# Performance work log

Hardware: AMD Instinct MI355X
Metric: run time of the kernel (lower is better)

The kernel has to match this reference:

```python
import jax, jax.numpy as jnp
import numpy as np

TOPK = 16  # module init arg
EPS = 1e-12  # F.normalize eps


def setup_inputs() -> dict:
    key = jax.random.key(0)
    k1, k2, k3 = jax.random.split(key, 3)
    b, c, h, w = 2, 256, 96, 96
    rc = max(c // 4, 16)  # reduced_channels = 64
    x = jax.random.normal(k1, (b, c, h, w), dtype=jnp.float32)
    # 1x1 convs are channel-mixing matmuls; store weights as [out_ch, in_ch]
    w_reduce = jax.random.normal(k2, (rc, c), dtype=jnp.float32) * 0.05
    w_proj = jax.random.normal(k3, (c, rc), dtype=jnp.float32) * 0.05
    return {"x": x, "w_reduce": w_reduce, "w_proj": w_proj}


def reference(x, w_reduce, w_proj):
    b, c, h, w = x.shape
    n = h * w
    # reduce: 1x1 conv == channel matmul -> [b, rc, N]
    feat = jnp.einsum('rc,bchw->brhw', w_reduce, x).reshape(b, -1, n)
    # F.normalize(dim=1): divide by max(L2-norm over channels, eps)
    nrm = jnp.maximum(jnp.sqrt(jnp.sum(feat * feat, axis=1, keepdims=True)), EPS)
    nf = jnp.transpose(feat / nrm, (0, 2, 1))  # [b, N, rc]
    # cosine similarity matrix [b, N, N]
    sim = jnp.einsum('bnr,bmr->bnm', nf, nf)
    k = min(TOPK, n)
    _, idx = jax.lax.top_k(sim, k)  # [b, N, k]
    # gather top-k neighbor features and average -> [b, N, rc]
    corr = jax.vmap(lambda f, i: f[i].mean(axis=1))(nf, idx)
    # proj: 1x1 conv back to C channels, NCHW layout
    enhanced = jnp.einsum('cr,bnr->bnc', w_proj, corr)
    enhanced = jnp.transpose(enhanced, (0, 2, 1)).reshape(b, c, h, w)
    return x + enhanced
```

## Files before the change

kernel.cpp:

```cpp
#include <hip/hip_runtime.h>
#include <cstdint>
#include <cstddef>

#define NPIX 9216
#define NB 2
#define NC 256
#define RC 64
#define TK 16
#define NROWS (NB * NPIX)
#define CT 128
#define ECOLS 1152
#define NTE 9
#define MAXC 128
#define MARGIN 0.008f

typedef unsigned short ushort_t;
typedef unsigned int uint_t;
typedef __bf16 bf16x8 __attribute__((ext_vector_type(8)));
typedef float f32x4 __attribute__((ext_vector_type(4)));

__device__ __forceinline__ uint_t f2bf(float x) {
  uint_t u = __float_as_uint(x);
  return (u + 0x7FFFu + ((u >> 16) & 1u)) >> 16;
}

__device__ __forceinline__ uint_t ordu(float v) {
  uint_t u = __float_as_uint(v);
  return (u & 0x80000000u) ? ~u : (u | 0x80000000u);
}

__global__ __launch_bounds__(256) void k_reduce(
    const float* __restrict__ x, const float* __restrict__ wr,
    float* __restrict__ feat4) {
  __shared__ float wl[64 * 16];
  const int bi = blockIdx.x;
  const int pg = bi >> 4, rq = (bi >> 2) & 3, cq = bi & 3;
  const int tid = threadIdx.x;
  {
    const int cl = tid >> 2, rg = (tid & 3) * 4;
#pragma unroll
    for (int i = 0; i < 4; ++i)
      wl[cl * 16 + rg + i] = wr[(size_t)(rq * 16 + rg + i) * NC + cq * 64 + cl];
  }
  __syncthreads();

  const int p = pg * 256 + tid;
  const int b = p >= NPIX;
  const int n = p - b * NPIX;
  const float* xp = x + (size_t)b * NC * NPIX + (size_t)cq * 64 * NPIX + n;

  float4 acc[4];
#pragma unroll
  for (int i = 0; i < 4; ++i) acc[i] = make_float4(0.f, 0.f, 0.f, 0.f);

  for (int c = 0; c < 64; ++c) {
    const float xv = xp[(size_t)c * NPIX];
    const float4* w4 = (const float4*)(wl + c * 16);
#pragma unroll
    for (int i = 0; i < 4; ++i) {
      float4 w = w4[i];
      acc[i].x += w.x * xv; acc[i].y += w.y * xv;
      acc[i].z += w.z * xv; acc[i].w += w.w * xv;
    }
  }
  float4* o = (float4*)(feat4 + (((size_t)(rq * 4 + cq)) * NROWS + p) * 16);
#pragma unroll
  for (int i = 0; i < 4; ++i) o[i] = acc[i];
}

__global__ __launch_bounds__(256) void k_normsplit(
    const float* __restrict__ feat4, float* __restrict__ nf,
    ushort_t* __restrict__ hi) {
  const int t = blockIdx.x * 256 + threadIdx.x;
  const int p = t >> 2, q = t & 3;
  float4 v[4];
#pragma unroll
  for (int i = 0; i < 4; ++i) v[i] = make_float4(0.f, 0.f, 0.f, 0.f);
#pragma unroll
  for (int pt = 0; pt < 4; ++pt) {
    const float4* fp = (const float4*)(feat4 + (((size_t)(q * 4 + pt)) * NROWS + p) * 16);
#pragma unroll
    for (int i = 0; i < 4; ++i) {
      float4 a = fp[i];
      v[i].x += a.x; v[i].y += a.y; v[i].z += a.z; v[i].w += a.w;
    }
  }
  float ssq = 0.f;
#pragma unroll
  for (int i = 0; i < 4; ++i)
    ssq += v[i].x * v[i].x + v[i].y * v[i].y + v[i].z * v[i].z + v[i].w * v[i].w;
  ssq += __shfl_xor(ssq, 1);
  ssq += __shfl_xor(ssq, 2);
  const float inv = 1.f / fmaxf(sqrtf(ssq), 1e-12f);

  float s[16];
#pragma unroll
  for (int i = 0; i < 4; ++i) {
    s[i * 4 + 0] = v[i].x * inv; s[i * 4 + 1] = v[i].y * inv;
    s[i * 4 + 2] = v[i].z * inv; s[i * 4 + 3] = v[i].w * inv;
  }
  float4* no = (float4*)(nf + (size_t)p * RC + q * 16);
#pragma unroll
  for (int i = 0; i < 4; ++i)
    no[i] = make_float4(s[i * 4], s[i * 4 + 1], s[i * 4 + 2], s[i * 4 + 3]);

  uint_t hs[16];
#pragma unroll
  for (int i = 0; i < 16; ++i) hs[i] = f2bf(s[i]);
  uint4* ho = (uint4*)(hi + (size_t)p * RC + q * 16);
#pragma unroll
  for (int h = 0; h < 2; ++h)
    ho[h] = make_uint4(hs[h*8+0] | (hs[h*8+1] << 16), hs[h*8+2] | (hs[h*8+3] << 16),
                       hs[h*8+4] | (hs[h*8+5] << 16), hs[h*8+6] | (hs[h*8+7] << 16));
}

__global__ __launch_bounds__(256) void k_sim_max(
    const ushort_t* __restrict__ nf_hi, float* __restrict__ tmax) {
  __shared__ ushort_t sh[CT * 72];
  const int rb = blockIdx.x >> 3, q = blockIdx.x & 7;
  const int tid = threadIdx.x, wave = tid >> 6, lane = tid & 63;
  const int n = lane & 15, quad = lane >> 4;
  const int r0 = rb * 128 + wave * 32 + n, r1 = r0 + 16;
  const int b = rb >= 72;
  const size_t cbase = (size_t)b * NPIX;

  const bf16x8 bh00 = *(const bf16x8*)(nf_hi + (size_t)r0 * 64 + quad * 8);
  const bf16x8 bh01 = *(const bf16x8*)(nf_hi + (size_t)r0 * 64 + 32 + quad * 8);
  const bf16x8 bh10 = *(const bf16x8*)(nf_hi + (size_t)r1 * 64 + quad * 8);
  const bf16x8 bh11 = *(const bf16x8*)(nf_hi + (size_t)r1 * 64 + 32 + quad * 8);

  const int sc = tid >> 1, sseg = (tid & 1) * 32;
  float cm0 = -1e30f, cm1 = -1e30f;

  for (int t = 0; t < NTE; ++t) {
    const int cb = q * ECOLS + t * CT;
    __syncthreads();
    {
      const uint4* g = (const uint4*)(nf_hi + (cbase + cb + sc) * 64 + sseg);
      uint4* d = (uint4*)(sh + sc * 72 + sseg);
#pragma unroll
      for (int i = 0; i < 4; ++i) d[i] = g[i];
    }
    __syncthreads();

#pragma unroll 2
    for (int st = 0; st < 8; ++st) {
      const ushort_t* ap = sh + (st * 16 + n) * 72 + quad * 8;
      bf16x8 ah0 = *(const bf16x8*)ap;
      bf16x8 ah1 = *(const bf16x8*)(ap + 32);
      f32x4 z = {0.f, 0.f, 0.f, 0.f};
      f32x4 a0 = __builtin_amdgcn_mfma_f32_16x16x32_bf16(ah0, bh00, z, 0, 0, 0);
      a0 = __builtin_amdgcn_mfma_f32_16x16x32_bf16(ah1, bh01, a0, 0, 0, 0);
      f32x4 a1 = __builtin_amdgcn_mfma_f32_16x16x32_bf16(ah0, bh10, z, 0, 0, 0);
      a1 = __builtin_amdgcn_mfma_f32_16x16x32_bf16(ah1, bh11, a1, 0, 0, 0);
      cm0 = fmaxf(cm0, fmaxf(fmaxf(a0[0], a0[1]), fmaxf(a0[2], a0[3])));
      cm1 = fmaxf(cm1, fmaxf(fmaxf(a1[0], a1[1]), fmaxf(a1[2], a1[3])));
    }
    if (t % 3 == 2) {
      const int cn = t / 3;
      tmax[(size_t)r0 * 96 + (q * 4 + quad) * 3 + cn] = cm0;
      tmax[(size_t)r1 * 96 + (q * 4 + quad) * 3 + cn] = cm1;
      cm0 = -1e30f; cm1 = -1e30f;
    }
  }
}

__global__ __launch_bounds__(256) void k_thresh(
    const float* __restrict__ tmax, float* __restrict__ Tb) {
  const int wave = threadIdx.x >> 6, lane = threadIdx.x & 63;
  const int row = blockIdx.x * 4 + wave;
  const float* tp = tmax + (size_t)row * 96;
  float v0 = tp[lane];
  float v1 = (lane < 32) ? tp[64 + lane] : -1e30f;
  float m = -1e30f;
#pragma unroll
  for (int k = 0; k < TK; ++k) {
    float c = fmaxf(v0, v1);
#pragma unroll
    for (int d = 1; d < 64; d <<= 1) c = fmaxf(c, __shfl_xor(c, d));
    m = c;
    if (v0 == m) v0 = -1e30f;
    if (v1 == m) v1 = -1e30f;
  }
  if (lane == 0) Tb[row] = m - MARGIN;
}

__global__ __launch_bounds__(256) void k_collect(
    const ushort_t* __restrict__ nf_hi, const float* __restrict__ Tb,
    int* __restrict__ cidx, int* __restrict__ rowcnt) {
  __shared__ ushort_t sh[CT * 72];
  const int rb = blockIdx.x >> 3, q = blockIdx.x & 7;
  const int tid = threadIdx.x, wave = tid >> 6, lane = tid & 63;
  const int n = lane & 15, quad = lane >> 4;
  const int r0 = rb * 128 + wave * 32 + n, r1 = r0 + 16;
  const int b = rb >= 72;
  const size_t cbase = (size_t)b * NPIX;

  const bf16x8 bh00 = *(const bf16x8*)(nf_hi + (size_t)r0 * 64 + quad * 8);
  const bf16x8 bh01 = *(const bf16x8*)(nf_hi + (size_t)r0 * 64 + 32 + quad * 8);
  const bf16x8 bh10 = *(const bf16x8*)(nf_hi + (size_t)r1 * 64 + quad * 8);
  const bf16x8 bh11 = *(const bf16x8*)(nf_hi + (size_t)r1 * 64 + 32 + quad * 8);

  const float T0 = Tb[r0], T1 = Tb[r1];
  const int sc = tid >> 1, sseg = (tid & 1) * 32;

  for (int t = 0; t < NTE; ++t) {
    const int cb = q * ECOLS + t * CT;
    __syncthreads();
    {
      const uint4* g = (const uint4*)(nf_hi + (cbase + cb + sc) * 64 + sseg);
      uint4* d = (uint4*)(sh + sc * 72 + sseg);
#pragma unroll
      for (int i = 0; i < 4; ++i) d[i] = g[i];
    }
    __syncthreads();

#pragma unroll 2
    for (int st = 0; st < 8; ++st) {
      const ushort_t* ap = sh + (st * 16 + n) * 72 + quad * 8;
      bf16x8 ah0 = *(const bf16x8*)ap;
      bf16x8 ah1 = *(const bf16x8*)(ap + 32);
      f32x4 z = {0.f, 0.f, 0.f, 0.f};
      f32x4 a0 = __builtin_amdgcn_mfma_f32_16x16x32_bf16(ah0, bh00, z, 0, 0, 0);
      a0 = __builtin_amdgcn_mfma_f32_16x16x32_bf16(ah1, bh01, a0, 0, 0, 0);
      f32x4 a1 = __builtin_amdgcn_mfma_f32_16x16x32_bf16(ah0, bh10, z, 0, 0, 0);
      a1 = __builtin_amdgcn_mfma_f32_16x16x32_bf16(ah1, bh11, a1, 0, 0, 0);

      const int c0 = cb + st * 16 + quad * 4;
      const float mx0 = fmaxf(fmaxf(a0[0], a0[1]), fmaxf(a0[2], a0[3]));
      if (mx0 >= T0) {
#pragma unroll
        for (int r = 0; r < 4; ++r)
          if (a0[r] >= T0) {
            const int slot = atomicAdd(rowcnt + r0, 1);
            if (slot < MAXC) cidx[(size_t)r0 * MAXC + slot] = c0 + r;
          }
      }
      const float mx1 = fmaxf(fmaxf(a1[0], a1[1]), fmaxf(a1[2], a1[3]));
      if (mx1 >= T1) {
#pragma unroll
        for (int r = 0; r < 4; ++r)
          if (a1[r] >= T1) {
            const int slot = atomicAdd(rowcnt + r1, 1);
            if (slot < MAXC) cidx[(size_t)r1 * MAXC + slot] = c0 + r;
          }
      }
    }
  }
}

__global__ __launch_bounds__(256) void k_merge_gather(
    const float* __restrict__ nf, const int* __restrict__ cidx,
    const int* __restrict__ rowcnt, float* __restrict__ corr) {
  const int wave = threadIdx.x >> 6, lane = threadIdx.x & 63;
  const int row0 = blockIdx.x * 16 + wave * 4;
#pragma unroll 1
  for (int rr = 0; rr < 4; ++rr) {
    const int row = row0 + rr;
    const int b = row >= NPIX;
    const int rl = row - b * NPIX;
    const float* nfb = nf + (size_t)b * NPIX * RC;
    const int C = min(rowcnt[row], MAXC);

    float4 rv[16];
    const float4* r4 = (const float4*)(nf + (size_t)row * RC);
#pragma unroll
    for (int i = 0; i < 16; ++i) rv[i] = r4[i];

    const int* cp = cidx + (size_t)row * MAXC;
    unsigned long long k0 = 0, k1 = 0;
    {
      const int c0 = (lane < C) ? cp[lane] : rl;
      const float4* g = (const float4*)(nfb + (size_t)c0 * RC);
      float s = 0.f;
#pragma unroll
      for (int i = 0; i < 16; ++i) {
        float4 a = g[i];
        s += a.x * rv[i].x + a.y * rv[i].y + a.z * rv[i].z + a.w * rv[i].w;
      }
      if (lane < C)
        k0 = ((unsigned long long)ordu(s) << 32) | (uint_t)(~(uint_t)c0);
    }
    if (C > 64) {
      const int c1 = (64 + lane < C) ? cp[64 + lane] : rl;
      const float4* g = (const float4*)(nfb + (size_t)c1 * RC);
      float s = 0.f;
#pragma unroll
      for (int i = 0; i < 16; ++i) {
        float4 a = g[i];
        s += a.x * rv[i].x + a.y * rv[i].y + a.z * rv[i].z + a.w * rv[i].w;
      }
      if (64 + lane < C)
        k1 = ((unsigned long long)ordu(s) << 32) | (uint_t)(~(uint_t)c1);
    }

    int sel[TK];
#pragma unroll
    for (int t = 0; t < TK; ++t) {
      unsigned long long m = k0 > k1 ? k0 : k1;
#pragma unroll
      for (int d = 1; d < 64; d <<= 1) {
        unsigned long long o = __shfl_xor(m, d);
        m = (o > m) ? o : m;
      }
      sel[t] = (m == 0) ? rl : (int)(~(uint_t)(m & 0xFFFFFFFFull));
      if (k0 == m) k0 = 0;
      else if (k1 == m) k1 = 0;
    }

    float acc = 0.f;
#pragma unroll
    for (int t = 0; t < TK; ++t)
      acc += nfb[(size_t)sel[t] * RC + lane];
    corr[(size_t)row * RC + lane] = acc * 0.0625f;
  }
}

__global__ __launch_bounds__(256) void k_proj_add(
    const float* __restrict__ x, const float* __restrict__ wp,
    const float* __restrict__ corr, float* __restrict__ out) {
  const int pg = blockIdx.x >> 3, cq = blockIdx.x & 7;
  const int tid = threadIdx.x;

  __shared__ float wl[32 * RC];
  {
    const float4* src = (const float4*)(wp + (size_t)cq * 32 * RC);
    float4* dst = (float4*)wl;
#pragma unroll
    for (int i = 0; i < 2; ++i) dst[i * 256 + tid] = src[i * 256 + tid];
  }

  const int p = pg * 256 + tid;
  const int b = p >= NPIX;
  const int n = p - b * NPIX;

  float4 cr[16];
  const float4* c4 = (const float4*)(corr + (size_t)p * RC);
#pragma unroll
  for (int i = 0; i < 16; ++i) cr[i] = c4[i];
  __syncthreads();

  const size_t xb = (size_t)b * NC * NPIX + n;
  for (int cl = 0; cl < 32; ++cl) {
    const float4* w4 = (const float4*)(wl + cl * RC);
    float s = 0.f;
#pragma unroll
    for (int i = 0; i < 16; ++i) {
      float4 w = w4[i];
      s += w.x * cr[i].x + w.y * cr[i].y + w.z * cr[i].z + w.w * cr[i].w;
    }
    const int c = cq * 32 + cl;
    const size_t oi = xb + (size_t)c * NPIX;
    out[oi] = x[oi] + s;
  }
}

extern "C" void kernel_launch(void* const* d_in, const int* in_sizes, int n_in,
                              void* d_out, int out_size, void* d_ws, size_t ws_size,
                              hipStream_t stream) {
  const float* x = (const float*)d_in[0];
  const float* wr = (const float*)d_in[1];
  const float* wp = (const float*)d_in[2];
  float* out = (float*)d_out;

  char* ws = (char*)d_ws;
  float* feat4 = (float*)ws;
  float* tmax = (float*)ws;
  float* corr = (float*)ws;
  float* nf = (float*)(ws + 18874368);
  ushort_t* nf_hi = (ushort_t*)(ws + 23592960);
  float* Tb = (float*)(ws + 25952256);
  int* rowcnt = (int*)(ws + 26025984);
  int* cidx = (int*)(ws + 26099712);

  hipLaunchKernelGGL(k_reduce, dim3(1152), dim3(256), 0, stream, x, wr, feat4);
  hipLaunchKernelGGL(k_normsplit, dim3(288), dim3(256), 0, stream, feat4, nf, nf_hi);
  hipLaunchKernelGGL(k_sim_max, dim3(1152), dim3(256), 0, stream, nf_hi, tmax);
  hipLaunchKernelGGL(k_thresh, dim3(NROWS / 4), dim3(256), 0, stream, tmax, Tb);
  hipMemsetAsync(rowcnt, 0, NROWS * sizeof(int), stream);
  hipLaunchKernelGGL(k_collect, dim3(1152), dim3(256), 0, stream,
                     nf_hi, Tb, cidx, rowcnt);
  hipLaunchKernelGGL(k_merge_gather, dim3(1152), dim3(256), 0, stream,
                     nf, cidx, rowcnt, corr);
  hipLaunchKernelGGL(k_proj_add, dim3(576), dim3(256), 0, stream, x, wp, corr, out);
}
```

Measured before the change: 311.6 us.

## Replace atomic candidate lists with per-stripe register buffers and drop LDS staging

k_collect no longer appends candidates through global atomics into a 128-slot list per row. Each lane keeps up to four candidates in registers for its own column stripe and writes them to a fixed slot, with a byte count. This removes the rowcnt memset and the atomics. k_sim_max and k_collect now read column tiles straight from global/L2 instead of staging them in LDS with barriers, and use twice as many blocks over 576-column slices, with 192 chunk maxima per row. k_reduce computes all 64 reduced channels per thread, with merge_gather handling one row per wave over 256 possible candidates. The risk is that the per-stripe cap of four drops true top-k neighbours when many cluster in one stripe.

```diff
diff --git a/kernel.cpp b/kernel.cpp
--- a/kernel.cpp
+++ b/kernel.cpp
@@ -8,13 +8,16 @@
 #define RC 64
 #define TK 16
 #define NROWS (NB * NPIX)
-#define CT 128
-#define ECOLS 1152
-#define NTE 9
-#define MAXC 128
+#define NQ 16
+#define ECOLS 576
+#define NSUB 36
+#define NCHK 192
+#define NSTR 64
+#define CAP 4
 #define MARGIN 0.008f
 
 typedef unsigned short ushort_t;
+typedef unsigned char uchar_t;
 typedef unsigned int uint_t;
 typedef __bf16 bf16x8 __attribute__((ext_vector_type(8)));
 typedef float f32x4 __attribute__((ext_vector_type(4)));
@@ -29,43 +32,43 @@
   return (u & 0x80000000u) ? ~u : (u | 0x80000000u);
 }
 
-__global__ __launch_bounds__(256) void k_reduce(
+__global__ __launch_bounds__(128) void k_reduce(
     const float* __restrict__ x, const float* __restrict__ wr,
     float* __restrict__ feat4) {
-  __shared__ float wl[64 * 16];
+  __shared__ float wl[64 * 64];
   const int bi = blockIdx.x;
-  const int pg = bi >> 4, rq = (bi >> 2) & 3, cq = bi & 3;
+  const int pg = bi >> 2, cq = bi & 3;
   const int tid = threadIdx.x;
-  {
-    const int cl = tid >> 2, rg = (tid & 3) * 4;
-#pragma unroll
-    for (int i = 0; i < 4; ++i)
-      wl[cl * 16 + rg + i] = wr[(size_t)(rq * 16 + rg + i) * NC + cq * 64 + cl];
+#pragma unroll
+  for (int i = 0; i < 32; ++i) {
+    const int idx = i * 128 + tid;
+    const int c = idx >> 6, r = idx & 63;
+    wl[c * 64 + r] = wr[(size_t)r * NC + cq * 64 + c];
   }
   __syncthreads();
 
-  const int p = pg * 256 + tid;
+  const int p = pg * 128 + tid;
   const int b = p >= NPIX;
   const int n = p - b * NPIX;
   const float* xp = x + (size_t)b * NC * NPIX + (size_t)cq * 64 * NPIX + n;
 
-  float4 acc[4];
-#pragma unroll
-  for (int i = 0; i < 4; ++i) acc[i] = make_float4(0.f, 0.f, 0.f, 0.f);
+  float4 acc[16];
+#pragma unroll
+  for (int i = 0; i < 16; ++i) acc[i] = make_float4(0.f, 0.f, 0.f, 0.f);
 
   for (int c = 0; c < 64; ++c) {
     const float xv = xp[(size_t)c * NPIX];
-    const float4* w4 = (const float4*)(wl + c * 16);
-#pragma unroll
-    for (int i = 0; i < 4; ++i) {
+    const float4* w4 = (const float4*)(wl + c * 64);
+#pragma unroll
+    for (int i = 0; i < 16; ++i) {
       float4 w = w4[i];
       acc[i].x += w.x * xv; acc[i].y += w.y * xv;
       acc[i].z += w.z * xv; acc[i].w += w.w * xv;
     }
   }
-  float4* o = (float4*)(feat4 + (((size_t)(rq * 4 + cq)) * NROWS + p) * 16);
-#pragma unroll
-  for (int i = 0; i < 4; ++i) o[i] = acc[i];
+  float4* o = (float4*)(feat4 + ((size_t)cq * NROWS + p) * 64);
+#pragma unroll
+  for (int i = 0; i < 16; ++i) o[i] = acc[i];
 }
 
 __global__ __launch_bounds__(256) void k_normsplit(
@@ -77,8 +80,8 @@
 #pragma unroll
   for (int i = 0; i < 4; ++i) v[i] = make_float4(0.f, 0.f, 0.f, 0.f);
 #pragma unroll
-  for (int pt = 0; pt < 4; ++pt) {
-    const float4* fp = (const float4*)(feat4 + (((size_t)(q * 4 + pt)) * NROWS + p) * 16);
+  for (int cq = 0; cq < 4; ++cq) {
+    const float4* fp = (const float4*)(feat4 + ((size_t)cq * NROWS + p) * 64 + q * 16);
 #pragma unroll
     for (int i = 0; i < 4; ++i) {
       float4 a = fp[i];
@@ -116,8 +119,7 @@
 
 __global__ __launch_bounds__(256) void k_sim_max(
     const ushort_t* __restrict__ nf_hi, float* __restrict__ tmax) {
-  __shared__ ushort_t sh[CT * 72];
-  const int rb = blockIdx.x >> 3, q = blockIdx.x & 7;
+  const int rb = blockIdx.x >> 4, q = blockIdx.x & 15;
   const int tid = threadIdx.x, wave = tid >> 6, lane = tid & 63;
   const int n = lane & 15, quad = lane >> 4;
   const int r0 = rb * 128 + wave * 32 + n, r1 = r0 + 16;
@@ -129,37 +131,25 @@
   const bf16x8 bh10 = *(const bf16x8*)(nf_hi + (size_t)r1 * 64 + quad * 8);
   const bf16x8 bh11 = *(const bf16x8*)(nf_hi + (size_t)r1 * 64 + 32 + quad * 8);
 
-  const int sc = tid >> 1, sseg = (tid & 1) * 32;
   float cm0 = -1e30f, cm1 = -1e30f;
 
-  for (int t = 0; t < NTE; ++t) {
-    const int cb = q * ECOLS + t * CT;
-    __syncthreads();
-    {
-      const uint4* g = (const uint4*)(nf_hi + (cbase + cb + sc) * 64 + sseg);
-      uint4* d = (uint4*)(sh + sc * 72 + sseg);
-#pragma unroll
-      for (int i = 0; i < 4; ++i) d[i] = g[i];
-    }
-    __syncthreads();
-
-#pragma unroll 2
-    for (int st = 0; st < 8; ++st) {
-      const ushort_t* ap = sh + (st * 16 + n) * 72 + quad * 8;
-      bf16x8 ah0 = *(const bf16x8*)ap;
-      bf16x8 ah1 = *(const bf16x8*)(ap + 32);
-      f32x4 z = {0.f, 0.f, 0.f, 0.f};
-      f32x4 a0 = __builtin_amdgcn_mfma_f32_16x16x32_bf16(ah0, bh00, z, 0, 0, 0);
-      a0 = __builtin_amdgcn_mfma_f32_16x16x32_bf16(ah1, bh01, a0, 0, 0, 0);
-      f32x4 a1 = __builtin_amdgcn_mfma_f32_16x16x32_bf16(ah0, bh10, z, 0, 0, 0);
-      a1 = __builtin_amdgcn_mfma_f32_16x16x32_bf16(ah1, bh11, a1, 0, 0, 0);
-      cm0 = fmaxf(cm0, fmaxf(fmaxf(a0[0], a0[1]), fmaxf(a0[2], a0[3])));
-      cm1 = fmaxf(cm1, fmaxf(fmaxf(a1[0], a1[1]), fmaxf(a1[2], a1[3])));
-    }
-    if (t % 3 == 2) {
-      const int cn = t / 3;
-      tmax[(size_t)r0 * 96 + (q * 4 + quad) * 3 + cn] = cm0;
-      tmax[(size_t)r1 * 96 + (q * 4 + quad) * 3 + cn] = cm1;
+#pragma unroll 6
+  for (int u = 0; u < NSUB; ++u) {
+    const int col = q * ECOLS + u * 16 + n;
+    const ushort_t* ap = nf_hi + (cbase + col) * 64 + quad * 8;
+    bf16x8 ah0 = *(const bf16x8*)ap;
+    bf16x8 ah1 = *(const bf16x8*)(ap + 32);
+    f32x4 z = {0.f, 0.f, 0.f, 0.f};
+    f32x4 a0 = __builtin_amdgcn_mfma_f32_16x16x32_bf16(ah0, bh00, z, 0, 0, 0);
+    a0 = __builtin_amdgcn_mfma_f32_16x16x32_bf16(ah1, bh01, a0, 0, 0, 0);
+    f32x4 a1 = __builtin_amdgcn_mfma_f32_16x16x32_bf16(ah0, bh10, z, 0, 0, 0);
+    a1 = __builtin_amdgcn_mfma_f32_16x16x32_bf16(ah1, bh11, a1, 0, 0, 0);
+    cm0 = fmaxf(cm0, fmaxf(fmaxf(a0[0], a0[1]), fmaxf(a0[2], a0[3])));
+    cm1 = fmaxf(cm1, fmaxf(fmaxf(a1[0], a1[1]), fmaxf(a1[2], a1[3])));
+    if ((u % 12) == 11) {
+      const int cn = (q * 4 + quad) * 3 + u / 12;
+      tmax[(size_t)r0 * NCHK + cn] = cm0;
+      tmax[(size_t)r1 * NCHK + cn] = cm1;
       cm0 = -1e30f; cm1 = -1e30f;
     }
   }
@@ -169,27 +159,28 @@
     const float* __restrict__ tmax, float* __restrict__ Tb) {
   const int wave = threadIdx.x >> 6, lane = threadIdx.x & 63;
   const int row = blockIdx.x * 4 + wave;
-  const float* tp = tmax + (size_t)row * 96;
+  const float* tp = tmax + (size_t)row * NCHK;
   float v0 = tp[lane];
-  float v1 = (lane < 32) ? tp[64 + lane] : -1e30f;
+  float v1 = tp[64 + lane];
+  float v2 = tp[128 + lane];
   float m = -1e30f;
 #pragma unroll
   for (int k = 0; k < TK; ++k) {
-    float c = fmaxf(v0, v1);
+    float c = fmaxf(fmaxf(v0, v1), v2);
 #pragma unroll
     for (int d = 1; d < 64; d <<= 1) c = fmaxf(c, __shfl_xor(c, d));
     m = c;
     if (v0 == m) v0 = -1e30f;
     if (v1 == m) v1 = -1e30f;
+    if (v2 == m) v2 = -1e30f;
   }
   if (lane == 0) Tb[row] = m - MARGIN;
 }
 
 __global__ __launch_bounds__(256) void k_collect(
     const ushort_t* __restrict__ nf_hi, const float* __restrict__ Tb,
-    int* __restrict__ cidx, int* __restrict__ rowcnt) {
-  __shared__ ushort_t sh[CT * 72];
-  const int rb = blockIdx.x >> 3, q = blockIdx.x & 7;
+    ushort_t* __restrict__ cidx2, uchar_t* __restrict__ cnt2) {
+  const int rb = blockIdx.x >> 4, q = blockIdx.x & 15;
   const int tid = threadIdx.x, wave = tid >> 6, lane = tid & 63;
   const int n = lane & 15, quad = lane >> 4;
   const int r0 = rb * 128 + wave * 32 + n, r1 = r0 + 16;
@@ -202,118 +193,106 @@
   const bf16x8 bh11 = *(const bf16x8*)(nf_hi + (size_t)r1 * 64 + 32 + quad * 8);
 
   const float T0 = Tb[r0], T1 = Tb[r1];
-  const int sc = tid >> 1, sseg = (tid & 1) * 32;
-
-  for (int t = 0; t < NTE; ++t) {
-    const int cb = q * ECOLS + t * CT;
-    __syncthreads();
-    {
-      const uint4* g = (const uint4*)(nf_hi + (cbase + cb + sc) * 64 + sseg);
-      uint4* d = (uint4*)(sh + sc * 72 + sseg);
-#pragma unroll
-      for (int i = 0; i < 4; ++i) d[i] = g[i];
-    }
-    __syncthreads();
-
-#pragma unroll 2
-    for (int st = 0; st < 8; ++st) {
-      const ushort_t* ap = sh + (st * 16 + n) * 72 + quad * 8;
-      bf16x8 ah0 = *(const bf16x8*)ap;
-      bf16x8 ah1 = *(const bf16x8*)(ap + 32);
-      f32x4 z = {0.f, 0.f, 0.f, 0.f};
-      f32x4 a0 = __builtin_amdgcn_mfma_f32_16x16x32_bf16(ah0, bh00, z, 0, 0, 0);
-      a0 = __builtin_amdgcn_mfma_f32_16x16x32_bf16(ah1, bh01, a0, 0, 0, 0);
-      f32x4 a1 = __builtin_amdgcn_mfma_f32_16x16x32_bf16(ah0, bh10, z, 0, 0, 0);
-      a1 = __builtin_amdgcn_mfma_f32_16x16x32_bf16(ah1, bh11, a1, 0, 0, 0);
-
-      const int c0 = cb + st * 16 + quad * 4;
-      const float mx0 = fmaxf(fmaxf(a0[0], a0[1]), fmaxf(a0[2], a0[3]));
-      if (mx0 >= T0) {
-#pragma unroll
-        for (int r = 0; r < 4; ++r)
-          if (a0[r] >= T0) {
-            const int slot = atomicAdd(rowcnt + r0, 1);
-            if (slot < MAXC) cidx[(size_t)r0 * MAXC + slot] = c0 + r;
-          }
-      }
-      const float mx1 = fmaxf(fmaxf(a1[0], a1[1]), fmaxf(a1[2], a1[3]));
-      if (mx1 >= T1) {
-#pragma unroll
-        for (int r = 0; r < 4; ++r)
-          if (a1[r] >= T1) {
-            const int slot = atomicAdd(rowcnt + r1, 1);
-            if (slot < MAXC) cidx[(size_t)r1 * MAXC + slot] = c0 + r;
-          }
-      }
-    }
-  }
+  ushort_t c0s[CAP], c1s[CAP];
+  int cnt0 = 0, cnt1 = 0;
+#pragma unroll
+  for (int i = 0; i < CAP; ++i) { c0s[i] = 0; c1s[i] = 0; }
+
+#pragma unroll 3
+  for (int u = 0; u < NSUB; ++u) {
+    const int col = q * ECOLS + u * 16 + n;
+    const ushort_t* ap = nf_hi + (cbase + col) * 64 + quad * 8;
+    bf16x8 ah0 = *(const bf16x8*)ap;
+    bf16x8 ah1 = *(const bf16x8*)(ap + 32);
+    f32x4 z = {0.f, 0.f, 0.f, 0.f};
+    f32x4 a0 = __builtin_amdgcn_mfma_f32_16x16x32_bf16(ah0, bh00, z, 0, 0, 0);
+    a0 = __builtin_amdgcn_mfma_f32_16x16x32_bf16(ah1, bh01, a0, 0, 0, 0);
+    f32x4 a1 = __builtin_amdgcn_mfma_f32_16x16x32_bf16(ah0, bh10, z, 0, 0, 0);
+    a1 = __builtin_amdgcn_mfma_f32_16x16x32_bf16(ah1, bh11, a1, 0, 0, 0);
+
+    const int c0 = q * ECOLS + u * 16 + quad * 4;
+    const float mx0 = fmaxf(fmaxf(a0[0], a0[1]), fmaxf(a0[2], a0[3]));
+    if (mx0 >= T0) {
+#pragma unroll
+      for (int r = 0; r < 4; ++r)
+        if (a0[r] >= T0 && cnt0 < CAP) { c0s[cnt0] = (ushort_t)(c0 + r); cnt0++; }
+    }
+    const float mx1 = fmaxf(fmaxf(a1[0], a1[1]), fmaxf(a1[2], a1[3]));
+    if (mx1 >= T1) {
+#pragma unroll
+      for (int r = 0; r < 4; ++r)
+        if (a1[r] >= T1 && cnt1 < CAP) { c1s[cnt1] = (ushort_t)(c0 + r); cnt1++; }
+    }
+  }
+
+  const int s0 = r0 * NSTR + q * 4 + quad, s1 = r1 * NSTR + q * 4 + quad;
+  *(ushort4*)(cidx2 + (size_t)s0 * CAP) =
+      make_ushort4(c0s[0], c0s[1], c0s[2], c0s[3]);
+  *(ushort4*)(cidx2 + (size_t)s1 * CAP) =
+      make_ushort4(c1s[0], c1s[1], c1s[2], c1s[3]);
+  cnt2[s0] = (uchar_t)cnt0;
+  cnt2[s1] = (uchar_t)cnt1;
 }
 
 __global__ __launch_bounds__(256) void k_merge_gather(
-    const float* __restrict__ nf, const int* __restrict__ cidx,
-    const int* __restrict__ rowcnt, float* __restrict__ corr) {
+    const float* __restrict__ nf, const ushort_t* __restrict__ cidx2,
+    const uchar_t* __restrict__ cnt2, float* __restrict__ corr) {
   const int wave = threadIdx.x >> 6, lane = threadIdx.x & 63;
-  const int row0 = blockIdx.x * 16 + wave * 4;
+  const int row = blockIdx.x * 4 + wave;
+  const int b = row >= NPIX;
+  const int rl = row - b * NPIX;
+  const float* nfb = nf + (size_t)b * NPIX * RC;
+
+  float4 rv[16];
+  const float4* r4 = (const float4*)(nf + (size_t)row * RC);
+#pragma unroll
+  for (int i = 0; i < 16; ++i) rv[i] = r4[i];
+
+  const int sidx = row * NSTR + lane;
+  const int cn = (int)cnt2[sidx];
+  const ushort4 cs = *(const ushort4*)(cidx2 + (size_t)sidx * CAP);
+  const ushort_t carr[CAP] = {cs.x, cs.y, cs.z, cs.w};
+
+  unsigned long long key[CAP];
+#pragma unroll
+  for (int j = 0; j < CAP; ++j) key[j] = 0;
 #pragma unroll 1
-  for (int rr = 0; rr < 4; ++rr) {
-    const int row = row0 + rr;
-    const int b = row >= NPIX;
-    const int rl = row - b * NPIX;
-    const float* nfb = nf + (size_t)b * NPIX * RC;
-    const int C = min(rowcnt[row], MAXC);
-
-    float4 rv[16];
-    const float4* r4 = (const float4*)(nf + (size_t)row * RC);
-#pragma unroll
-    for (int i = 0; i < 16; ++i) rv[i] = r4[i];
-
-    const int* cp = cidx + (size_t)row * MAXC;
-    unsigned long long k0 = 0, k1 = 0;
-    {
-      const int c0 = (lane < C) ? cp[lane] : rl;
-      const float4* g = (const float4*)(nfb + (size_t)c0 * RC);
+  for (int j = 0; j < CAP; ++j) {
+    if (j < cn) {
+      const int c = (int)carr[j];
+      const float4* g = (const float4*)(nfb + (size_t)c * RC);
       float s = 0.f;
 #pragma unroll
       for (int i = 0; i < 16; ++i) {
         float4 a = g[i];
         s += a.x * rv[i].x + a.y * rv[i].y + a.z * rv[i].z + a.w * rv[i].w;
       }
-      if (lane < C)
-        k0 = ((unsigned long long)ordu(s) << 32) | (uint_t)(~(uint_t)c0);
-    }
-    if (C > 64) {
-      const int c1 = (64 + lane < C) ? cp[64 + lane] : rl;
-      const float4* g = (const float4*)(nfb + (size_t)c1 * RC);
-      float s = 0.f;
-#pragma unroll
-      for (int i = 0; i < 16; ++i) {
-        float4 a = g[i];
-        s += a.x * rv[i].x + a.y * rv[i].y + a.z * rv[i].z + a.w * rv[i].w;
-      }
-      if (64 + lane < C)
-        k1 = ((unsigned long long)ordu(s) << 32) | (uint_t)(~(uint_t)c1);
-    }
-
-    int sel[TK];
-#pragma unroll
-    for (int t = 0; t < TK; ++t) {
-      unsigned long long m = k0 > k1 ? k0 : k1;
-#pragma unroll
-      for (int d = 1; d < 64; d <<= 1) {
-        unsigned long long o = __shfl_xor(m, d);
-        m = (o > m) ? o : m;
-      }
-      sel[t] = (m == 0) ? rl : (int)(~(uint_t)(m & 0xFFFFFFFFull));
-      if (k0 == m) k0 = 0;
-      else if (k1 == m) k1 = 0;
-    }
-
-    float acc = 0.f;
-#pragma unroll
-    for (int t = 0; t < TK; ++t)
-      acc += nfb[(size_t)sel[t] * RC + lane];
-    corr[(size_t)row * RC + lane] = acc * 0.0625f;
-  }
+      key[j] = ((unsigned long long)ordu(s) << 32) | (uint_t)(~(uint_t)c);
+    }
+  }
+
+  int sel[TK];
+#pragma unroll
+  for (int t = 0; t < TK; ++t) {
+    unsigned long long m = key[0];
+#pragma unroll
+    for (int j = 1; j < CAP; ++j) m = key[j] > m ? key[j] : m;
+#pragma unroll
+    for (int d = 1; d < 64; d <<= 1) {
+      unsigned long long o = __shfl_xor(m, d);
+      m = (o > m) ? o : m;
+    }
+    sel[t] = (m == 0) ? rl : (int)(~(uint_t)(m & 0xFFFFFFFFull));
+#pragma unroll
+    for (int j = 0; j < CAP; ++j)
+      if (key[j] == m) key[j] = 0;
+  }
+
+  float acc = 0.f;
+#pragma unroll
+  for (int t = 0; t < TK; ++t)
+    acc += nfb[(size_t)sel[t] * RC + lane];
+  corr[(size_t)row * RC + lane] = acc * 0.0625f;
 }
 
 __global__ __launch_bounds__(256) void k_proj_add(
@@ -370,17 +349,16 @@
   float* nf = (float*)(ws + 18874368);
   ushort_t* nf_hi = (ushort_t*)(ws + 23592960);
   float* Tb = (float*)(ws + 25952256);
-  int* rowcnt = (int*)(ws + 26025984);
-  int* cidx = (int*)(ws + 26099712);
-
-  hipLaunchKernelGGL(k_reduce, dim3(1152), dim3(256), 0, stream, x, wr, feat4);
+  uchar_t* cnt2 = (uchar_t*)(ws + 26025984);
+  ushort_t* cidx2 = (ushort_t*)(ws + 27205632);
+
+  hipLaunchKernelGGL(k_reduce, dim3(576), dim3(128), 0, stream, x, wr, feat4);
   hipLaunchKernelGGL(k_normsplit, dim3(288), dim3(256), 0, stream, feat4, nf, nf_hi);
-  hipLaunchKernelGGL(k_sim_max, dim3(1152), dim3(256), 0, stream, nf_hi, tmax);
+  hipLaunchKernelGGL(k_sim_max, dim3(2304), dim3(256), 0, stream, nf_hi, tmax);
   hipLaunchKernelGGL(k_thresh, dim3(NROWS / 4), dim3(256), 0, stream, tmax, Tb);
-  hipMemsetAsync(rowcnt, 0, NROWS * sizeof(int), stream);
-  hipLaunchKernelGGL(k_collect, dim3(1152), dim3(256), 0, stream,
-                     nf_hi, Tb, cidx, rowcnt);
-  hipLaunchKernelGGL(k_merge_gather, dim3(1152), dim3(256), 0, stream,
-                     nf, cidx, rowcnt, corr);
+  hipLaunchKernelGGL(k_collect, dim3(2304), dim3(256), 0, stream,
+                     nf_hi, Tb, cidx2, cnt2);
+  hipLaunchKernelGGL(k_merge_gather, dim3(NROWS / 4), dim3(256), 0, stream,
+                     nf, cidx2, cnt2, corr);
   hipLaunchKernelGGL(k_proj_add, dim3(576), dim3(256), 0, stream, x, wp, corr, out);
 }
```

Result: slower. 399.8 us (+28.3%).
